# Performance work log

Measured on AMD Instinct MI355X. Metric: run time of the kernel, lower is better.

Reference implementation:

```python
import jax, jax.numpy as jnp
import numpy as np

N, B, M, C, NH, S, HC, T, OUT = 8, 256, 512, 512, 8, 8, 64, 3, 100
DH = C // NH


def setup_inputs() -> dict:
    key = jax.random.key(0)
    it = iter(jax.random.split(key, 40))
    def nrm(shape, s=0.02):
        return jax.random.normal(next(it), shape, jnp.float32) * s
    z = lambda shape: jnp.zeros(shape, jnp.float32)
    return {
        "x": jax.random.normal(next(it), (B, 3, 32, 32), jnp.float32),
        "conv1_w": nrm((N, 64, 3, 3, 3)), "conv1_b": z((N, 64)),
        "conv2_w": nrm((N, 128, 64, 3, 3)), "conv2_b": z((N, 128)),
        "feat_w": nrm((N, 128, M)), "feat_b": z((N, M)),
        "ctrl_wi": nrm((N, M, 3 * HC)), "ctrl_wh": nrm((N, HC, 3 * HC)),
        "ctrl_bi": z((N, 3 * HC)), "ctrl_bh": z((N, 3 * HC)),
        "send_w": nrm((N, HC, 1)), "send_b": z((N, 1)),
        "recv_w": nrm((N, HC, 1)), "recv_b": z((N, 1)),
        "abias_w": nrm((N, HC, NH)), "abias_b": z((N, NH)),
        "wq": nrm((N, M, C)), "wk": nrm((N, M, C)), "wv": nrm((N, M, C)),
        "wo": nrm((N, C, C)), "bo": z((N, C)),
        "edge_logits": nrm((N, N), 0.1),
        "wr": nrm((N, C, M)), "br": z((N, M)),
        "wg": nrm((N, 3 * M, M)), "bg": z((N, M)),
        "wc": nrm((N, 3 * M, M)), "bc": z((N, M)),
        "wcls": nrm((N, M, OUT)), "bcls": z((N, OUT)),
    }


def _forward(x, conv1_w, conv1_b, conv2_w, conv2_b, feat_w, feat_b,
             ctrl_wi, ctrl_wh, ctrl_bi, ctrl_bh,
             send_w, send_b, recv_w, recv_b, abias_w, abias_b,
             wq, wk, wv, wo, bo, edge_logits, wr, br,
             wg, bg, wc, bc, wcls, bcls):
    dn = ('NCHW', 'OIHW', 'NCHW')
    def conv(inp, w, b):
        y = jax.lax.conv_general_dilated(inp, w, (2, 2), 'SAME', dimension_numbers=dn)
        return jax.nn.relu(y + b[None, :, None, None])
    # per-node feature extraction (batched over N experts via vmap)
    h1 = jax.vmap(lambda w, b: conv(x, w, b))(conv1_w, conv1_b)          # [N,B,64,16,16]
    h2 = jax.vmap(conv, in_axes=(0, 0, 0))(h1, conv2_w, conv2_b)        # [N,B,128,8,8]
    pooled = h2.mean(axis=(-2, -1))                                      # [N,B,128]
    feats = jax.nn.relu(jnp.einsum('nbf,nfm->nbm', pooled, feat_w) + feat_b[:, None, :])
    h = feats                                                            # node states [N,B,M]
    cs = jnp.zeros((N, B, HC), x.dtype)                                  # controller GRU states
    buf = jnp.zeros((N, B, S, C), x.dtype)                               # message buffers
    scale = 1.0 / jnp.sqrt(jnp.asarray(DH, x.dtype))
    for t in range(T):
        # controller (GRUCell) -> send/recv gates + per-head attention bias
        gi = jnp.einsum('nbm,nmh->nbh', h, ctrl_wi) + ctrl_bi[:, None, :]
        gh = jnp.einsum('nbh,nhk->nbk', cs, ctrl_wh) + ctrl_bh[:, None, :]
        iz, ir, inn = jnp.split(gi, 3, -1)
        hz, hr, hn = jnp.split(gh, 3, -1)
        zg = jax.nn.sigmoid(iz + hz)
        rg = jax.nn.sigmoid(ir + hr)
        ng = jnp.tanh(inn + rg * hn)
        cs = (1.0 - zg) * ng + zg * cs
        send = jax.nn.sigmoid(jnp.einsum('nbh,nho->nbo', cs, send_w) + send_b[:, None, :])  # [N,B,1]
        recv = jax.nn.sigmoid(jnp.einsum('nbh,nho->nbo', cs, recv_w) + recv_b[:, None, :])  # [N,B,1]
        ab = jnp.einsum('nbh,nhk->nbk', cs, abias_w) + abias_b[:, None, :]                  # [N,B,NH]
        # per-node QKV
        q = jnp.einsum('nbm,nmc->nbc', h, wq).reshape(N, B, NH, DH)
        k = jnp.einsum('nbm,nmc->nbc', h, wk).reshape(N, B, NH, DH)
        v = jnp.einsum('nbm,nmc->nbc', h, wv).reshape(N, B, NH, DH)
        # graph-transformer attention over nodes: i=receiver, j=sender
        scores = jnp.einsum('ibhd,jbhd->ijbh', q, k) * scale
        scores = scores + edge_logits[:, :, None, None] + ab[:, None, :, :]
        attn = jax.nn.softmax(scores, axis=1)
        attn = attn * send[None, :, :, :] * recv[:, None, :, :]          # gated [N,N,B,NH]
        msg = jnp.einsum('ijbh,jbhd->ibhd', attn, v).reshape(N, B, C)
        msg = jnp.einsum('nbc,nck->nbk', msg, wo) + bo[:, None, :]
        # push into FIFO buffer, read out mean
        buf = jnp.concatenate([buf[:, :, 1:], msg[:, :, None, :]], axis=2)
        readout = jnp.einsum('nbc,ncm->nbm', buf.mean(axis=2), wr) + br[:, None, :]
        # gated state update fusing h, fresh features, buffer readout
        cat = jnp.concatenate([h, feats, readout], axis=-1)              # [N,B,3M]
        g = jax.nn.sigmoid(jnp.einsum('nbk,nkm->nbm', cat, wg) + bg[:, None, :])
        cand = jnp.tanh(jnp.einsum('nbk,nkm->nbm', cat, wc) + bc[:, None, :])
        h = (1.0 - g) * h + g * cand
    logits = jnp.einsum('nbm,nmo->nbo', h, wcls) + bcls[:, None, :]      # [N,B,OUT]
    return logits


def reference(x, conv1_w, conv1_b, conv2_w, conv2_b, feat_w, feat_b,
              ctrl_wi, ctrl_wh, ctrl_bi, ctrl_bh,
              send_w, send_b, recv_w, recv_b, abias_w, abias_b,
              wq, wk, wv, wo, bo, edge_logits, wr, br,
              wg, bg, wc, bc, wcls, bcls):
    return _forward(x, conv1_w, conv1_b, conv2_w, conv2_b, feat_w, feat_b,
                    ctrl_wi, ctrl_wh, ctrl_bi, ctrl_bh,
                    send_w, send_b, recv_w, recv_b, abias_w, abias_b,
                    wq, wk, wv, wo, bo, edge_logits, wr, br,
                    wg, bg, wc, bc, wcls, bcls)
```

## Files before the change

kernel.cpp:

```cpp
#include <hip/hip_runtime.h>
#include <hip/hip_bf16.h>


typedef _Float16 f16;
typedef _Float16 f16x8 __attribute__((ext_vector_type(8)));
typedef _Float16 f16x4 __attribute__((ext_vector_type(4)));
typedef _Float16 f16x2 __attribute__((ext_vector_type(2)));
typedef float f32x4 __attribute__((ext_vector_type(4)));

#define GLOAD_LDS16(gsrc, ldst)                                                   \
  __builtin_amdgcn_global_load_lds(                                               \
      (const __attribute__((address_space(1))) void*)(gsrc),                      \
      (__attribute__((address_space(3))) void*)(ldst), 16, 0, 0)

__device__ __forceinline__ void tw64_body(
    const float* __restrict__ s, f16* __restrict__ d, int K, int N, float scale,
    int n0, int k0, int t)
{
  __shared__ float tile[64][65];
#pragma unroll
  for (int p = 0; p < 4; p++) {
    int idx = t + p * 256;
    int kk = idx >> 4, nq = (idx & 15) * 4;
    float4 v = *(const float4*)&s[(long)(k0 + kk) * N + n0 + nq];
    tile[kk][nq] = v.x; tile[kk][nq + 1] = v.y; tile[kk][nq + 2] = v.z; tile[kk][nq + 3] = v.w;
  }
  __syncthreads();
#pragma unroll
  for (int p = 0; p < 2; p++) {
    int idx = t + p * 256;
    int nn = idx >> 3, kc = (idx & 7) * 8;
    f16 o[8];
#pragma unroll
    for (int i = 0; i < 8; i++) o[i] = (f16)(tile[kc + i][nn] * scale);
    *(f16x8*)&d[(long)(n0 + nn) * K + k0 + kc] = *(const f16x8*)o;
  }
}

__global__ __launch_bounds__(256) void tw64_kernel(
    const float* __restrict__ src, f16* __restrict__ dst, int K, int N, float scale)
{
  int z = blockIdx.z;
  tw64_body(src + (long)z * K * N, dst + (long)z * N * K, K, N, scale,
            blockIdx.x * 64, blockIdx.y * 64, threadIdx.x);
}

__global__ __launch_bounds__(256) void twmulti4_kernel(
    const float* __restrict__ wq, const float* __restrict__ wk,
    const float* __restrict__ wv, const float* __restrict__ wi, f16* __restrict__ wqT)
{
  int z = blockIdx.z, sel = z >> 3, e = z & 7;
  int N = (sel < 3) ? 512 : 192;
  int n0 = blockIdx.x * 64;
  if (n0 >= N) return;
  const float* src = (sel == 0) ? wq : (sel == 1) ? wk : (sel == 2) ? wv : wi;
  f16* dst = (sel < 3) ? (wqT + (long)sel * 2097152 + (long)e * 262144)
                       : (wqT + 3L * 2097152 + (long)e * 98304);
  tw64_body(src + (long)e * 512 * N, dst, 512, N, 1.f, n0, blockIdx.y * 64, threadIdx.x);
}

__global__ __launch_bounds__(256) void twmulti2_kernel(
    const float* __restrict__ wg, const float* __restrict__ wc, f16* __restrict__ wgT)
{
  int z = blockIdx.z, sel = z >> 3, e = z & 7;
  const float* src = sel ? wc : wg;
  f16* dst = wgT + (long)sel * 6291456 + (long)e * 786432;
  tw64_body(src + (long)e * 1536 * 512, dst, 1536, 512, 1.f,
            blockIdx.x * 64, blockIdx.y * 64, threadIdx.x);
}

__global__ __launch_bounds__(256) void clsprep_kernel(
    const float* __restrict__ wcls, f16* __restrict__ wclsT)
{
  __shared__ float tile[32][33];
  int e = blockIdx.z;
  int n0 = blockIdx.x * 32, k0 = blockIdx.y * 32;
  int tx = threadIdx.x & 31, ty = threadIdx.x >> 5;
  const float* s = wcls + (long)e * 51200;
  f16* d = wclsT + (long)e * 65536;
  for (int r = ty; r < 32; r += 8) {
    int k = k0 + r, n = n0 + tx;
    tile[r][tx] = (n < 100) ? s[(long)k * 100 + n] : 0.f;
  }
  __syncthreads();
  for (int r = ty; r < 32; r += 8) {
    int n = n0 + r, k = k0 + tx;
    d[(long)n * 512 + k] = (f16)tile[tx][r];
  }
}

__global__ __launch_bounds__(256) void smallprep_kernel(
    const float* __restrict__ wo, f16* __restrict__ wo16,
    const float* __restrict__ c2src, f16* __restrict__ c2dst,
    const float* __restrict__ w1src, f16* __restrict__ w1dst)
{
  int bid = blockIdx.x, t = threadIdx.x;
  if (bid < 1024) {
    long i = ((long)bid * 256 + t) * 8;
    float4 a = *(const float4*)&wo[i];
    float4 b = *(const float4*)&wo[i + 4];
    f16 o[8] = {(f16)a.x, (f16)a.y, (f16)a.z, (f16)a.w, (f16)b.x, (f16)b.y, (f16)b.z, (f16)b.w};
    *(f16x8*)&wo16[i] = *(const f16x8*)o;
  } else if (bid < 3328) {
    long i = (long)(bid - 1024) * 256 + t;
    int ci = i & 63; long r = i >> 6; int tap = r % 9; r /= 9; int co = r & 127; int n = (int)(r >> 7);
    c2dst[i] = (f16)c2src[(((long)(n * 128 + co) * 64 + ci) * 9) + tap];
  } else {
    int i = (bid - 3328) * 256 + t;
    int j = i & 7, co = (i >> 3) & 63, slot = (i >> 9) & 3, e = i >> 11;
    int k = slot * 8 + j;
    w1dst[i] = (f16)((k < 27) ? w1src[(long)e * 1728 + co * 27 + k] : 0.f);
  }
}

__global__ __launch_bounds__(256) void xprep_kernel(
    const float* __restrict__ x, f16* __restrict__ xp16)
{
  __shared__ float xs[3072];
  int b = blockIdx.x, t = threadIdx.x;
  const float* xb = x + (long)b * 3072;
  for (int i = t; i < 768; i += 256) ((float4*)xs)[i] = ((const float4*)xb)[i];
  __syncthreads();
  int oy = t >> 4, ox = t & 15;
  f16 pv[32];
#pragma unroll
  for (int q = 27; q < 32; q++) pv[q] = (f16)0.f;
#pragma unroll
  for (int ci = 0; ci < 3; ci++)
#pragma unroll
    for (int ky = 0; ky < 3; ky++) {
      int iy = oy * 2 + ky;
#pragma unroll
      for (int kx = 0; kx < 3; kx++) {
        int ix = ox * 2 + kx;
        pv[ci * 9 + ky * 3 + kx] =
            (f16)((iy < 32 && ix < 32) ? xs[ci * 1024 + iy * 32 + ix] : 0.f);
      }
    }
  f16* ob = xp16 + (long)b * 8192;
#pragma unroll
  for (int c = 0; c < 4; c++) *(f16x8*)&ob[c * 2048 + t * 8] = *(const f16x8*)&pv[c * 8];
}

__global__ __launch_bounds__(256) void borprep2_kernel(
    const f16* __restrict__ wrT, const float* __restrict__ bo, float* __restrict__ bor32)
{
  int n = blockIdx.y, t = threadIdx.x;
  int og = blockIdx.x * 16 + (t >> 4), k16 = t & 15;
  const f16* row = wrT + (long)n * 262144 + (long)og * 512 + k16 * 32;
  const float* bp = bo + n * 512 + k16 * 32;
  float s = 0.f;
#pragma unroll
  for (int i = 0; i < 32; i += 8) {
    f16x8 v = *(const f16x8*)&row[i];
    float4 b0 = *(const float4*)&bp[i];
    float4 b1 = *(const float4*)&bp[i + 4];
    s = fmaf((float)v[0], b0.x, s); s = fmaf((float)v[1], b0.y, s);
    s = fmaf((float)v[2], b0.z, s); s = fmaf((float)v[3], b0.w, s);
    s = fmaf((float)v[4], b1.x, s); s = fmaf((float)v[5], b1.y, s);
    s = fmaf((float)v[6], b1.z, s); s = fmaf((float)v[7], b1.w, s);
  }
  s += __shfl_xor(s, 1); s += __shfl_xor(s, 2);
  s += __shfl_xor(s, 4); s += __shfl_xor(s, 8);
  if (k16 == 0) bor32[n * 512 + og] = s;
}

__global__ __launch_bounds__(256) void biasfold2_kernel(
    const f16* __restrict__ wgT, const f16* __restrict__ wcT,
    const float* __restrict__ bg, const float* __restrict__ bc,
    const float* __restrict__ br, const float* __restrict__ bor32,
    float* __restrict__ bgr, float* __restrict__ vg2,
    float* __restrict__ bcr, float* __restrict__ vc2)
{
  int n = blockIdx.y, t = threadIdx.x;
  int og = blockIdx.x * 16 + (t >> 4), k16 = t & 15;
  const f16* gr = wgT + (long)n * 786432 + (long)og * 1536 + 1024 + k16 * 32;
  const f16* cr = wcT + (long)n * 786432 + (long)og * 1536 + 1024 + k16 * 32;
  const float* brp = br + n * 512 + k16 * 32;
  const float* bop = bor32 + n * 512 + k16 * 32;
  float s1g = 0.f, s2g = 0.f, s1c = 0.f, s2c = 0.f;
#pragma unroll
  for (int i = 0; i < 32; i += 8) {
    f16x8 gv = *(const f16x8*)&gr[i];
    f16x8 cv = *(const f16x8*)&cr[i];
#pragma unroll
    for (int q = 0; q < 8; q++) {
      float brm = brp[i + q], bom = bop[i + q];
      s1g = fmaf(brm, (float)gv[q], s1g); s2g = fmaf(bom, (float)gv[q], s2g);
      s1c = fmaf(brm, (float)cv[q], s1c); s2c = fmaf(bom, (float)cv[q], s2c);
    }
  }
#pragma unroll
  for (int o = 1; o < 16; o <<= 1) {
    s1g += __shfl_xor(s1g, o); s2g += __shfl_xor(s2g, o);
    s1c += __shfl_xor(s1c, o); s2c += __shfl_xor(s2c, o);
  }
  if (k16 == 0) {
    bgr[n * 512 + og] = bg[n * 512 + og] + s1g; vg2[n * 512 + og] = s2g;
    bcr[n * 512 + og] = bc[n * 512 + og] + s1c; vc2[n * 512 + og] = s2c;
  }
}

__global__ __launch_bounds__(256) void convfused_kernel(
    const f16* __restrict__ xp16, const f16* __restrict__ w1p, const float* __restrict__ b1,
    const f16* __restrict__ w2p, const float* __restrict__ b2, f16* __restrict__ pooled16)
{
  __shared__ __align__(16) char lds[53632];
  f16* xpatch = (f16*)lds;
  f16* AsubS = (f16*)lds;
  float* red = (float*)lds;
  float* bs1 = (float*)(lds + 16384);
  f16* h1s = (f16*)(lds + 16640);
  f16* ws1 = (f16*)(lds + 16640);

  int b = blockIdx.x, e = blockIdx.y;
  int t = threadIdx.x, w = t >> 6, l = t & 63;

  const f16* xb = xp16 + (long)b * 8192;
#pragma unroll
  for (int c = 0; c < 4; c++)
    GLOAD_LDS16(xb + (w * 4 + c) * 512 + l * 8, &xpatch[(w * 4 + c) * 512]);
  GLOAD_LDS16(w1p + (long)e * 2048 + w * 512 + l * 8, &ws1[w * 512]);
  if (t < 64) bs1[t] = b1[e * 64 + t];
  asm volatile("s_waitcnt vmcnt(0)" ::: "memory");
  __syncthreads();

  {
    int pw = w * 64;
    f16x8 a1[4], b1f[4];
#pragma unroll
    for (int i = 0; i < 4; i++)
      a1[i] = *(const f16x8*)&ws1[(l >> 4) * 512 + (i * 16 + (l & 15)) * 8];
#pragma unroll
    for (int jj = 0; jj < 4; jj++)
      b1f[jj] = *(const f16x8*)&xpatch[(l >> 4) * 2048 + (pw + jj * 16 + (l & 15)) * 8];
    __syncthreads();
    f32x4 acc1[4][4];
#pragma unroll
    for (int i = 0; i < 4; i++)
#pragma unroll
      for (int jj = 0; jj < 4; jj++)
        acc1[i][jj] = __builtin_amdgcn_mfma_f32_16x16x32_f16(
            a1[i], b1f[jj], (f32x4){0.f, 0.f, 0.f, 0.f}, 0, 0, 0);
#pragma unroll
    for (int i = 0; i < 4; i++) {
      int co0 = i * 16 + ((l >> 4) << 2);
      float bi0 = bs1[co0], bi1 = bs1[co0 + 1], bi2 = bs1[co0 + 2], bi3 = bs1[co0 + 3];
#pragma unroll
      for (int jj = 0; jj < 4; jj++) {
        int p2 = pw + jj * 16 + (l & 15);
        int oy2 = p2 >> 4, ox2 = p2 & 15;
        int p = oy2 * 17 + ox2;
        int fs = ((ox2 >> 1) + oy2) & 7;
        int slot = (co0 >> 3) ^ fs;
        f16x4 v;
        v[0] = (f16)fmaxf(acc1[i][jj][0] + bi0, 0.f);
        v[1] = (f16)fmaxf(acc1[i][jj][1] + bi1, 0.f);
        v[2] = (f16)fmaxf(acc1[i][jj][2] + bi2, 0.f);
        v[3] = (f16)fmaxf(acc1[i][jj][3] + bi3, 0.f);
        *(f16x4*)&h1s[p * 64 + slot * 8 + (co0 & 7)] = v;
      }
    }
  }
  if (t < 33) {
    int gy = (t < 17) ? 16 : (t - 17);
    int gx = (t < 17) ? t : 16;
    int p = gy * 17 + gx;
    f16x8 zz = {};
#pragma unroll
    for (int g = 0; g < 8; g++) *(f16x8*)&h1s[p * 64 + g * 8] = zz;
  }

  int waveR = w >> 1, waveC = w & 1;
  const f16* wbase = w2p + (long)e * 73728;
  f32x4 acc[4][2];
#pragma unroll
  for (int i = 0; i < 4; i++) {
    acc[i][0] = (f32x4){0.f, 0.f, 0.f, 0.f};
    acc[i][1] = (f32x4){0.f, 0.f, 0.f, 0.f};
  }
  for (int tap = 0; tap < 9; tap++) {
    __syncthreads();
#pragma unroll
    for (int c = 0; c < 4; c++) {
      int ch = w * 4 + c;
      int co = ch * 8 + (l >> 3);
      int g = (l & 7) ^ (co & 7);
      GLOAD_LDS16(wbase + ((long)co * 9 + tap) * 64 + g * 8, &AsubS[ch * 512]);
    }
    asm volatile("s_waitcnt vmcnt(0)" ::: "memory");
    __syncthreads();
    int ky = tap / 3, kx = tap - ky * 3;
#pragma unroll
    for (int kk = 0; kk < 2; kk++) {
      f16x8 af[4], bf[2];
#pragma unroll
      for (int i = 0; i < 4; i++) {
        int row = waveR * 64 + i * 16 + (l & 15);
        int blk = (kk * 4 + (l >> 4)) ^ (row & 7);
        af[i] = *(const f16x8*)&AsubS[row * 64 + blk * 8];
      }
#pragma unroll
      for (int j = 0; j < 2; j++) {
        int sp = waveC * 32 + j * 16 + (l & 15);
        int iy = (sp >> 3) * 2 + ky, ix = (sp & 7) * 2 + kx;
        int fs = ((ix >> 1) + iy) & 7;
        int blk = (kk * 4 + (l >> 4)) ^ fs;
        bf[j] = *(const f16x8*)&h1s[(iy * 17 + ix) * 64 + blk * 8];
      }
#pragma unroll
      for (int i = 0; i < 4; i++)
#pragma unroll
        for (int j = 0; j < 2; j++)
          acc[i][j] = __builtin_amdgcn_mfma_f32_16x16x32_f16(af[i], bf[j], acc[i][j], 0, 0, 0);
    }
  }
  __syncthreads();
  const float* bn2 = b2 + e * 128;
#pragma unroll
  for (int i = 0; i < 4; i++) {
#pragma unroll
    for (int reg = 0; reg < 4; reg++) {
      int row = waveR * 64 + i * 16 + ((l >> 4) << 2) + reg;
      float bi = bn2[row];
      float s = fmaxf(acc[i][0][reg] + bi, 0.f) + fmaxf(acc[i][1][reg] + bi, 0.f);
      s += __shfl_xor(s, 1); s += __shfl_xor(s, 2);
      s += __shfl_xor(s, 4); s += __shfl_xor(s, 8);
      if ((l & 15) == 0) red[waveC * 128 + row] = s;
    }
  }
  __syncthreads();
  if (t < 128) {
    float v = (red[t] + red[128 + t]) * (1.f / 64.f);
    pooled16[((long)e * 256 + b) * 128 + t] = (f16)v;
  }
}

struct SegsM {
  const f16* BT[4];
  const float* bias[4];
  f16* o16[4];
  f16* o16b[4];
  float* o32[4];
  long sBT[4], sBias[4], sO16[4], sO32[4];
  int ldo16[4], ldo32[4], act[4], segCols[4];
};

template <int MR>
__global__ __launch_bounds__(256) void gemmf16_kernel(
    const f16* __restrict__ A, long sA, int lda, SegsM segs, int K)
{
  constexpr int IW = MR / 32;
  __shared__ __align__(16) f16 Asub[2][MR * 64];
  __shared__ __align__(16) f16 Bsub[2][4096];
  int z = blockIdx.z;
  int rowBase = blockIdx.y * MR;
  int vcBase = blockIdx.x * 64;
  int seg = vcBase >> 9;
  int lcBase = vcBase & 511;
  const f16* An = A + (long)z * sA + (long)rowBase * lda;
  const f16* BTn = segs.BT[seg] + (long)z * segs.sBT[seg] + (long)lcBase * K;
  const float* biasN = segs.bias[seg] ? segs.bias[seg] + (long)z * segs.sBias[seg] : nullptr;
  int act = segs.act[seg];
  int segCols = segs.segCols[seg];
  int t = threadIdx.x, w = t >> 6, l = t & 63;
  int waveR = w >> 1, waveC = w & 1;
  f32x4 acc[IW][2];
#pragma unroll
  for (int i = 0; i < IW; i++) {
    acc[i][0] = (f32x4){0.f, 0.f, 0.f, 0.f};
    acc[i][1] = (f32x4){0.f, 0.f, 0.f, 0.f};
  }
  auto stage = [&](int buf, int kt) {
    int k0 = kt << 6;
#pragma unroll
    for (int c = 0; c < MR / 32; c++) {
      int ch = w * (MR / 32) + c;
      int row = ch * 8 + (l >> 3);
      int g = (l & 7) ^ (row & 7);
      GLOAD_LDS16(An + (long)row * lda + k0 + g * 8, &Asub[buf][ch * 512]);
    }
#pragma unroll
    for (int c = 0; c < 2; c++) {
      int ch = w * 2 + c;
      int col = ch * 8 + (l >> 3);
      int g = (l & 7) ^ (col & 7);
      GLOAD_LDS16(BTn + (long)col * K + k0 + g * 8, &Bsub[buf][ch * 512]);
    }
  };
  int nk = K >> 6;
  stage(0, 0);
  asm volatile("s_waitcnt vmcnt(0)" ::: "memory");
  __syncthreads();
  int cur = 0;
  for (int kt = 0; kt < nk; kt++) {
    if (kt + 1 < nk) stage(cur ^ 1, kt + 1);
#pragma unroll
    for (int kk = 0; kk < 2; kk++) {
      f16x8 af[IW], bf[2];
#pragma unroll
      for (int i = 0; i < IW; i++) {
        int row = waveR * (MR / 2) + i * 16 + (l & 15);
        int blk = (kk * 4 + (l >> 4)) ^ (row & 7);
        af[i] = *(const f16x8*)&Asub[cur][row * 64 + blk * 8];
      }
#pragma unroll
      for (int j = 0; j < 2; j++) {
        int col = waveC * 32 + j * 16 + (l & 15);
        int blk = (kk * 4 + (l >> 4)) ^ (col & 7);
        bf[j] = *(const f16x8*)&Bsub[cur][col * 64 + blk * 8];
      }
#pragma unroll
      for (int i = 0; i < IW; i++)
#pragma unroll
        for (int j = 0; j < 2; j++)
          acc[i][j] = __builtin_amdgcn_mfma_f32_16x16x32_f16(af[i], bf[j], acc[i][j], 0, 0, 0);
    }
    if (kt + 1 < nk) {
      asm volatile("s_waitcnt vmcnt(0)" ::: "memory");
      __syncthreads();
      cur ^= 1;
    }
  }
  f16* o16 = segs.o16[seg];
  f16* o16b = segs.o16b[seg];
  float* o32 = segs.o32[seg];
  long sO16 = segs.sO16[seg], sO32 = segs.sO32[seg];
  int ldo16 = segs.ldo16[seg], ldo32 = segs.ldo32[seg];
#pragma unroll
  for (int i = 0; i < IW; i++) {
    int rb = rowBase + waveR * (MR / 2) + i * 16 + ((l >> 4) << 2);
#pragma unroll
    for (int j = 0; j < 2; j++) {
      int lc = lcBase + waveC * 32 + j * 16 + (l & 15);
      if (lc >= segCols) continue;
      float bv = biasN ? biasN[lc] : 0.f;
#pragma unroll
      for (int reg = 0; reg < 4; reg++) {
        float v = acc[i][j][reg] + bv;
        if (act == 1) v = fmaxf(v, 0.f);
        else if (act == 2) v = 1.f / (1.f + __expf(-v));
        else if (act == 3) v = tanhf(v);
        long rr = rb + reg;
        if (o16) o16[(long)z * sO16 + rr * ldo16 + lc] = (f16)v;
        if (o16b) o16b[(long)z * sO16 + rr * ldo16 + lc] = (f16)v;
        if (o32) o32[(long)z * sO32 + rr * ldo32 + lc] = v;
      }
    }
  }
}

__global__ __launch_bounds__(256) void step_kernel(
    const f16* __restrict__ qkv16, const float* __restrict__ gi32,
    const float* __restrict__ wh, const float* __restrict__ bh,
    float* __restrict__ cs, const float* __restrict__ sw, const float* __restrict__ sb,
    const float* __restrict__ rw, const float* __restrict__ rb,
    const float* __restrict__ aw, const float* __restrict__ abb,
    const float* __restrict__ edge,
    float* __restrict__ msgsum32, f16* __restrict__ msgsum16, int step)
{
  int b = blockIdx.x, t = threadIdx.x;
  __shared__ float qs[8 * 520], ks[8 * 520];
  __shared__ f16 vs16[8 * 520];
  __shared__ float csh[512];
  __shared__ float sc[512];
  __shared__ float se[8], re[8], edg[64], abl[64];

  for (int i = t; i < 2048; i += 256) {
    int nn = i >> 8, c2 = (i & 255) * 2;
    int h = c2 >> 6, d = c2 & 63;
    long base = ((long)nn * 256 + b) * 1536 + c2;
    int la = nn * 520 + h * 65 + d;
    f16x2 qv = *(const f16x2*)&qkv16[base];
    f16x2 kv = *(const f16x2*)&qkv16[base + 512];
    *(f16x2*)&vs16[la] = *(const f16x2*)&qkv16[base + 1024];
    qs[la] = (float)qv[0]; qs[la + 1] = (float)qv[1];
    ks[la] = (float)kv[0]; ks[la + 1] = (float)kv[1];
  }
  if (t >= 192) edg[t - 192] = edge[t - 192];
  int n0 = t >> 6, hc = t & 63;
  if (step > 0) {
    csh[t] = cs[((long)n0 * 256 + b) * 64 + hc];
    csh[t + 256] = cs[((long)(n0 + 4) * 256 + b) * 64 + hc];
  }
  __syncthreads();

  float cn[2];
#pragma unroll
  for (int u = 0; u < 2; u++) {
    int n = n0 + u * 4;
    long nb = (long)n * 256 + b;
    float c0 = (step > 0) ? csh[n * 64 + hc] : 0.f;
    float g0 = bh[n * 192 + hc], g1 = bh[n * 192 + 64 + hc], g2 = bh[n * 192 + 128 + hc];
    if (step > 0) {
      const float* whn = wh + (long)n * 12288;
      for (int k = 0; k < 64; k++) {
        float cv = csh[n * 64 + k];
        g0 = fmaf(cv, whn[k * 192 + hc], g0);
        g1 = fmaf(cv, whn[k * 192 + 64 + hc], g1);
        g2 = fmaf(cv, whn[k * 192 + 128 + hc], g2);
      }
    }
    const float* gi = gi32 + nb * 192;
    float zg = 1.f / (1.f + __expf(-(gi[hc] + g0)));
    float rg = 1.f / (1.f + __expf(-(gi[64 + hc] + g1)));
    float ng = tanhf(gi[128 + hc] + rg * g2);
    cn[u] = (1.f - zg) * ng + zg * c0;
    cs[nb * 64 + hc] = cn[u];
  }
#pragma unroll
  for (int u = 0; u < 2; u++) {
    int n = n0 + u * 4;
    float ps = cn[u] * sw[n * 64 + hc];
    float pr = cn[u] * rw[n * 64 + hc];
#pragma unroll
    for (int o = 32; o; o >>= 1) { ps += __shfl_xor(ps, o); pr += __shfl_xor(pr, o); }
    if (hc == 0) {
      se[n] = 1.f / (1.f + __expf(-(ps + sb[n])));
      re[n] = 1.f / (1.f + __expf(-(pr + rb[n])));
    }
#pragma unroll
    for (int kk = 0; kk < 8; kk++) {
      float pa = cn[u] * aw[(n * 64 + hc) * 8 + kk];
#pragma unroll
      for (int o = 32; o; o >>= 1) pa += __shfl_xor(pa, o);
      if (hc == 0) abl[n * 8 + kk] = pa + abb[n * 8 + kk];
    }
  }
  __syncthreads();

  for (int idx = t; idx < 512; idx += 256) {
    int i = idx >> 6, j = (idx >> 3) & 7, h = idx & 7;
    const float* qp = &qs[i * 520 + h * 65];
    const float* kp = &ks[j * 520 + h * 65];
    float s = 0.f;
#pragma unroll
    for (int d = 0; d < 64; d++) s = fmaf(qp[d], kp[d], s);
    sc[idx] = s * 0.125f + edg[i * 8 + j] + abl[i * 8 + h];
  }
  __syncthreads();
  if (t < 64) {
    int i = t >> 3, h = t & 7;
    float mx = -1e30f;
#pragma unroll
    for (int j = 0; j < 8; j++) mx = fmaxf(mx, sc[(i << 6) + (j << 3) + h]);
    float e[8], sm = 0.f;
#pragma unroll
    for (int j = 0; j < 8; j++) { e[j] = __expf(sc[(i << 6) + (j << 3) + h] - mx); sm += e[j]; }
    float inv = re[i] / sm;
#pragma unroll
    for (int j = 0; j < 8; j++) sc[(i << 6) + (j << 3) + h] = e[j] * inv * se[j];
  }
  __syncthreads();
  for (int idx = t; idx < 4096; idx += 256) {
    int i = idx >> 9, c = idx & 511, h = c >> 6, d = c & 63;
    float s = 0.f;
#pragma unroll
    for (int j = 0; j < 8; j++)
      s = fmaf(sc[(i << 6) + (j << 3) + h], (float)vs16[j * 520 + h * 65 + d], s);
    long oi = ((long)i * 256 + b) * 512 + c;
    float nv = (step == 0) ? s : (msgsum32[oi] + s);
    msgsum32[oi] = nv;
    msgsum16[oi] = (f16)nv;
  }
}

__global__ __launch_bounds__(256) void gatefused_kernel(
    const f16* __restrict__ h16cur, const f16* __restrict__ feats16,
    const f16* __restrict__ msgsum16,
    const f16* __restrict__ wgT, const f16* __restrict__ wcT,
    const f16* __restrict__ WeffGT, const f16* __restrict__ WeffCT,
    const float* __restrict__ bgr, const float* __restrict__ vg2,
    const float* __restrict__ bcr, const float* __restrict__ vc2,
    float* __restrict__ h32, f16* __restrict__ h16next, float tp1)
{
  __shared__ __align__(16) f16 Asub[2][2048];
  __shared__ __align__(16) f16 Bgs[2][4096];
  __shared__ __align__(16) f16 Bcs[2][4096];
  int z = blockIdx.z;
  int rowBase = blockIdx.y * 32;
  int colBase = blockIdx.x * 64;
  int t = threadIdx.x, w = t >> 6, l = t & 63;
  int waveR = w >> 1, waveC = w & 1;
  f32x4 accG[2], accC[2];
  accG[0] = (f32x4){0.f, 0.f, 0.f, 0.f}; accG[1] = accG[0];
  accC[0] = accG[0]; accC[1] = accG[0];

  auto stage = [&](int buf, int kt) {
    {
      const f16* asrc;
      if (kt < 8)       asrc = h16cur  + (long)z * 131072 + kt * 64;
      else if (kt < 16) asrc = feats16 + (long)z * 131072 + (kt - 8) * 64;
      else              asrc = msgsum16 + (long)z * 131072 + (kt - 16) * 64;
      int row = w * 8 + (l >> 3);
      int g = (l & 7) ^ (row & 7);
      GLOAD_LDS16(asrc + (long)(rowBase + row) * 512 + g * 8, &Asub[buf][w * 512]);
    }
#pragma unroll
    for (int c = 0; c < 2; c++) {
      int ch = w * 2 + c;
      int cl = ch * 8 + (l >> 3);
      int g = (l & 7) ^ (cl & 7);
      const f16 *bgsrc, *bcsrc;
      if (kt < 16) {
        bgsrc = wgT + (long)z * 786432 + (long)(colBase + cl) * 1536 + kt * 64 + g * 8;
        bcsrc = wcT + (long)z * 786432 + (long)(colBase + cl) * 1536 + kt * 64 + g * 8;
      } else {
        bgsrc = WeffGT + (long)z * 262144 + (long)(colBase + cl) * 512 + (kt - 16) * 64 + g * 8;
        bcsrc = WeffCT + (long)z * 262144 + (long)(colBase + cl) * 512 + (kt - 16) * 64 + g * 8;
      }
      GLOAD_LDS16(bgsrc, &Bgs[buf][ch * 512]);
      GLOAD_LDS16(bcsrc, &Bcs[buf][ch * 512]);
    }
  };
  stage(0, 0);
  asm volatile("s_waitcnt vmcnt(0)" ::: "memory");
  __syncthreads();
  int cur = 0;
  for (int kt = 0; kt < 24; kt++) {
    if (kt + 1 < 24) stage(cur ^ 1, kt + 1);
#pragma unroll
    for (int kk = 0; kk < 2; kk++) {
      f16x8 af, bgf[2], bcf[2];
      {
        int row = waveR * 16 + (l & 15);
        int blk = (kk * 4 + (l >> 4)) ^ (row & 7);
        af = *(const f16x8*)&Asub[cur][row * 64 + blk * 8];
      }
#pragma unroll
      for (int j = 0; j < 2; j++) {
        int cl = waveC * 32 + j * 16 + (l & 15);
        int blk = (kk * 4 + (l >> 4)) ^ (cl & 7);
        bgf[j] = *(const f16x8*)&Bgs[cur][cl * 64 + blk * 8];
        bcf[j] = *(const f16x8*)&Bcs[cur][cl * 64 + blk * 8];
      }
#pragma unroll
      for (int j = 0; j < 2; j++) {
        accG[j] = __builtin_amdgcn_mfma_f32_16x16x32_f16(af, bgf[j], accG[j], 0, 0, 0);
        accC[j] = __builtin_amdgcn_mfma_f32_16x16x32_f16(af, bcf[j], accC[j], 0, 0, 0);
      }
    }
    if (kt + 1 < 24) {
      asm volatile("s_waitcnt vmcnt(0)" ::: "memory");
      __syncthreads();
      cur ^= 1;
    }
  }
#pragma unroll
  for (int j = 0; j < 2; j++) {
    int col = colBase + waveC * 32 + j * 16 + (l & 15);
    float bG = bgr[z * 512 + col] + tp1 * vg2[z * 512 + col];
    float bC = bcr[z * 512 + col] + tp1 * vc2[z * 512 + col];
#pragma unroll
    for (int reg = 0; reg < 4; reg++) {
      int row = rowBase + waveR * 16 + ((l >> 4) << 2) + reg;
      float g = 1.f / (1.f + __expf(-(accG[j][reg] + bG)));
      float cd = tanhf(accC[j][reg] + bC);
      long hidx = ((long)z * 256 + row) * 512 + col;
      float h = h32[hidx];
      float nh = (1.f - g) * h + g * cd;
      h32[hidx] = nh;
      h16next[hidx] = (f16)nh;
    }
  }
}

extern "C" void kernel_launch(void* const* d_in, const int* in_sizes, int n_in,
                              void* d_out, int out_size, void* d_ws, size_t ws_size,
                              hipStream_t stream)
{
  (void)in_sizes; (void)n_in; (void)out_size;
  const float* x        = (const float*)d_in[0];
  const float* conv1_w  = (const float*)d_in[1];
  const float* conv1_b  = (const float*)d_in[2];
  const float* conv2_w  = (const float*)d_in[3];
  const float* conv2_b  = (const float*)d_in[4];
  const float* feat_w   = (const float*)d_in[5];
  const float* feat_b   = (const float*)d_in[6];
  const float* ctrl_wi  = (const float*)d_in[7];
  const float* ctrl_wh  = (const float*)d_in[8];
  const float* ctrl_bi  = (const float*)d_in[9];
  const float* ctrl_bh  = (const float*)d_in[10];
  const float* send_w   = (const float*)d_in[11];
  const float* send_b   = (const float*)d_in[12];
  const float* recv_w   = (const float*)d_in[13];
  const float* recv_b   = (const float*)d_in[14];
  const float* abias_w  = (const float*)d_in[15];
  const float* abias_b  = (const float*)d_in[16];
  const float* wq       = (const float*)d_in[17];
  const float* wk       = (const float*)d_in[18];
  const float* wv       = (const float*)d_in[19];
  const float* wo       = (const float*)d_in[20];
  const float* bo       = (const float*)d_in[21];
  const float* edge     = (const float*)d_in[22];
  const float* wr       = (const float*)d_in[23];
  const float* br       = (const float*)d_in[24];
  const float* wg       = (const float*)d_in[25];
  const float* bg       = (const float*)d_in[26];
  const float* wc       = (const float*)d_in[27];
  const float* bc       = (const float*)d_in[28];
  const float* wcls     = (const float*)d_in[29];
  const float* bcls     = (const float*)d_in[30];

  float* f32b = (float*)d_ws;
  float* h32      = f32b;
  float* gi32     = f32b + 1048576;
  float* msgsum32 = f32b + 1441792;
  float* cs       = f32b + 2490368;
  float* bor32    = f32b + 2621440;
  float* bgr      = f32b + 2625536;
  float* vg2b     = f32b + 2629632;
  float* bcr      = f32b + 2633728;
  float* vc2b     = f32b + 2637824;
  f16* hb = (f16*)(f32b + 2641920);
  f16* pooled16 = hb;
  f16* h16a     = hb + 262144;
  f16* h16b     = hb + 1310720;
  f16* feats16  = hb + 2359296;
  f16* msgsum16 = hb + 3407872;
  f16* qkv16    = hb + 4456448;
  f16* wqT      = hb + 7602176;
  f16* wiT      = hb + 13893632;
  f16* featwT   = hb + 14680064;
  f16* wrT      = hb + 15204352;
  f16* wgT      = hb + 17301504;
  f16* wcT      = hb + 23592960;
  f16* c2wp     = hb + 29884416;
  f16* wo16     = hb + 30474240;
  f16* P        = hb + 32571392;
  f16* P2       = hb + 34668544;
  f16* WeffGT   = hb + 36765696;
  f16* WeffCT   = hb + 38862848;
  f16* w1p      = hb + 40960000;
  f16* xp16     = hb + 40976384;
  f16* wclsT    = hb + 43073536;
  if (ws_size < 97763328ull) return;

  f16* hbuf[2] = {h16a, h16b};

  twmulti4_kernel<<<dim3(8, 8, 32), 256, 0, stream>>>(wq, wk, wv, ctrl_wi, wqT);
  twmulti2_kernel<<<dim3(8, 24, 16), 256, 0, stream>>>(wg, wc, wgT);
  tw64_kernel<<<dim3(8, 8, 8), 256, 0, stream>>>(wr, wrT, 512, 512, 0.125f);
  tw64_kernel<<<dim3(8, 2, 8), 256, 0, stream>>>(feat_w, featwT, 128, 512, 1.f);
  smallprep_kernel<<<3392, 256, 0, stream>>>(wo, wo16, conv2_w, c2wp, conv1_w, w1p);
  xprep_kernel<<<256, 256, 0, stream>>>(x, xp16);
  clsprep_kernel<<<dim3(4, 16, 8), 256, 0, stream>>>(wcls, wclsT);
  borprep2_kernel<<<dim3(32, 8), 256, 0, stream>>>(wrT, bo, bor32);
  biasfold2_kernel<<<dim3(32, 8), 256, 0, stream>>>(wgT, wcT, bg, bc, br, bor32,
                                                    bgr, vg2b, bcr, vc2b);
  {
    SegsM s{};
    s.BT[0] = wrT; s.sBT[0] = 262144;
    s.o16[0] = P; s.o16b[0] = P2; s.sO16[0] = 262144; s.ldo16[0] = 512;
    s.segCols[0] = 512;
    gemmf16_kernel<64><<<dim3(8, 8, 8), 256, 0, stream>>>(wo16, 262144L, 512, s, 512);
  }
  {
    SegsM s{};
    s.BT[0] = P; s.sBT[0] = 262144;
    s.o16[0] = WeffGT; s.sO16[0] = 262144; s.ldo16[0] = 512;
    s.segCols[0] = 512;
    gemmf16_kernel<64><<<dim3(8, 8, 16), 256, 0, stream>>>(wgT + 1024, 786432L, 1536, s, 512);
  }

  convfused_kernel<<<dim3(256, 8), 256, 0, stream>>>(xp16, w1p, conv1_b, c2wp, conv2_b, pooled16);

  {
    SegsM s{};
    s.BT[0] = featwT; s.sBT[0] = 65536; s.bias[0] = feat_b; s.sBias[0] = 512; s.act[0] = 1;
    s.o16[0] = feats16; s.o16b[0] = h16a; s.sO16[0] = 131072; s.ldo16[0] = 512;
    s.o32[0] = h32; s.sO32[0] = 131072; s.ldo32[0] = 512;
    s.segCols[0] = 512;
    gemmf16_kernel<128><<<dim3(8, 2, 8), 256, 0, stream>>>(pooled16, 32768L, 128, s, 128);
  }

  for (int step = 0; step < 3; step++) {
    {
      SegsM s{};
      s.BT[0] = wqT;            s.sBT[0] = 262144;
      s.BT[1] = wqT + 2097152;  s.sBT[1] = 262144;
      s.BT[2] = wqT + 4194304;  s.sBT[2] = 262144;
      s.BT[3] = wiT;            s.sBT[3] = 98304;
      s.bias[3] = ctrl_bi; s.sBias[3] = 192;
      s.o16[0] = qkv16;        s.sO16[0] = 393216; s.ldo16[0] = 1536;
      s.o16[1] = qkv16 + 512;  s.sO16[1] = 393216; s.ldo16[1] = 1536;
      s.o16[2] = qkv16 + 1024; s.sO16[2] = 393216; s.ldo16[2] = 1536;
      s.o32[3] = gi32; s.sO32[3] = 49152; s.ldo32[3] = 192;
      s.segCols[0] = 512; s.segCols[1] = 512; s.segCols[2] = 512; s.segCols[3] = 192;
      gemmf16_kernel<128><<<dim3(27, 2, 8), 256, 0, stream>>>(hbuf[step & 1], 131072L, 512, s, 512);
    }
    step_kernel<<<256, 256, 0, stream>>>(
        qkv16, gi32, ctrl_wh, ctrl_bh, cs, send_w, send_b, recv_w, recv_b,
        abias_w, abias_b, edge, msgsum32, msgsum16, step);
    gatefused_kernel<<<dim3(8, 8, 8), 256, 0, stream>>>(
        hbuf[step & 1], feats16, msgsum16, wgT, wcT, WeffGT, WeffCT,
        bgr, vg2b, bcr, vc2b, h32, hbuf[(step + 1) & 1], (float)(step + 1));
  }
  {
    SegsM s{};
    s.BT[0] = wclsT; s.sBT[0] = 65536;
    s.bias[0] = bcls; s.sBias[0] = 100;
    s.o32[0] = (float*)d_out; s.sO32[0] = 25600; s.ldo32[0] = 100;
    s.segCols[0] = 100;
    gemmf16_kernel<128><<<dim3(2, 2, 8), 256, 0, stream>>>(hbuf[1], 131072L, 512, s, 512);
  }
}
```

Baseline: 324.2 us.

## Split conv2 output channels across blocks and triple-buffer weight taps

The fused conv kernel now launches twice as many blocks, each computing 64 of the 128 conv2 output channels and recomputing conv1 for its image. Conv1 weights and input are read straight from global into registers instead of through LDS. Conv2 weight taps are triple-buffered in LDS with partial vmcnt waits, so the next taps load while the current one computes, and there is one barrier per tap instead of two. This trades doubled conv1 work for more parallelism and load/compute overlap, with a larger LDS footprint per block.

```diff
diff --git a/kernel.cpp b/kernel.cpp
--- a/kernel.cpp
+++ b/kernel.cpp
@@ -205,36 +205,40 @@
     const f16* __restrict__ xp16, const f16* __restrict__ w1p, const float* __restrict__ b1,
     const f16* __restrict__ w2p, const float* __restrict__ b2, f16* __restrict__ pooled16)
 {
-  __shared__ __align__(16) char lds[53632];
-  f16* xpatch = (f16*)lds;
-  f16* AsubS = (f16*)lds;
+  __shared__ __align__(16) char lds[61568];
+  f16* Asub = (f16*)lds;
   float* red = (float*)lds;
-  float* bs1 = (float*)(lds + 16384);
-  f16* h1s = (f16*)(lds + 16640);
-  f16* ws1 = (f16*)(lds + 16640);
-
-  int b = blockIdx.x, e = blockIdx.y;
+  f16* h1s = (f16*)(lds + 24576);
+
+  int b = blockIdx.x, e = blockIdx.y, ch2 = blockIdx.z;
   int t = threadIdx.x, w = t >> 6, l = t & 63;
-
-  const f16* xb = xp16 + (long)b * 8192;
-#pragma unroll
-  for (int c = 0; c < 4; c++)
-    GLOAD_LDS16(xb + (w * 4 + c) * 512 + l * 8, &xpatch[(w * 4 + c) * 512]);
-  GLOAD_LDS16(w1p + (long)e * 2048 + w * 512 + l * 8, &ws1[w * 512]);
-  if (t < 64) bs1[t] = b1[e * 64 + t];
-  asm volatile("s_waitcnt vmcnt(0)" ::: "memory");
-  __syncthreads();
+  int waveR = w >> 1, waveC = w & 1;
+
+  const f16* wsg = w1p + (long)e * 2048;
+  const f16* xg = xp16 + (long)b * 8192;
+  int pw = w * 64;
+  f16x8 a1[4], b1f[4];
+#pragma unroll
+  for (int i = 0; i < 4; i++)
+    a1[i] = *(const f16x8*)&wsg[(l >> 4) * 512 + (i * 16 + (l & 15)) * 8];
+#pragma unroll
+  for (int jj = 0; jj < 4; jj++)
+    b1f[jj] = *(const f16x8*)&xg[(l >> 4) * 2048 + (pw + jj * 16 + (l & 15)) * 8];
+
+  const f16* wbase = w2p + (long)e * 73728 + (long)ch2 * 36864;
+  auto stageA = [&](int buf, int tap) {
+#pragma unroll
+    for (int c = 0; c < 2; c++) {
+      int ch = w * 2 + c;
+      int row = ch * 8 + (l >> 3);
+      int g = (l & 7) ^ (row & 7);
+      GLOAD_LDS16(wbase + (long)row * 576 + tap * 64 + g * 8, &Asub[buf * 4096 + ch * 512]);
+    }
+  };
+  stageA(0, 0);
+  stageA(1, 1);
 
   {
-    int pw = w * 64;
-    f16x8 a1[4], b1f[4];
-#pragma unroll
-    for (int i = 0; i < 4; i++)
-      a1[i] = *(const f16x8*)&ws1[(l >> 4) * 512 + (i * 16 + (l & 15)) * 8];
-#pragma unroll
-    for (int jj = 0; jj < 4; jj++)
-      b1f[jj] = *(const f16x8*)&xpatch[(l >> 4) * 2048 + (pw + jj * 16 + (l & 15)) * 8];
-    __syncthreads();
     f32x4 acc1[4][4];
 #pragma unroll
     for (int i = 0; i < 4; i++)
@@ -245,7 +249,7 @@
 #pragma unroll
     for (int i = 0; i < 4; i++) {
       int co0 = i * 16 + ((l >> 4) << 2);
-      float bi0 = bs1[co0], bi1 = bs1[co0 + 1], bi2 = bs1[co0 + 2], bi3 = bs1[co0 + 3];
+      float4 bv = *(const float4*)&b1[e * 64 + co0];
 #pragma unroll
       for (int jj = 0; jj < 4; jj++) {
         int p2 = pw + jj * 16 + (l & 15);
@@ -254,10 +258,10 @@
         int fs = ((ox2 >> 1) + oy2) & 7;
         int slot = (co0 >> 3) ^ fs;
         f16x4 v;
-        v[0] = (f16)fmaxf(acc1[i][jj][0] + bi0, 0.f);
-        v[1] = (f16)fmaxf(acc1[i][jj][1] + bi1, 0.f);
-        v[2] = (f16)fmaxf(acc1[i][jj][2] + bi2, 0.f);
-        v[3] = (f16)fmaxf(acc1[i][jj][3] + bi3, 0.f);
+        v[0] = (f16)fmaxf(acc1[i][jj][0] + bv.x, 0.f);
+        v[1] = (f16)fmaxf(acc1[i][jj][1] + bv.y, 0.f);
+        v[2] = (f16)fmaxf(acc1[i][jj][2] + bv.z, 0.f);
+        v[3] = (f16)fmaxf(acc1[i][jj][3] + bv.w, 0.f);
         *(f16x4*)&h1s[p * 64 + slot * 8 + (co0 & 7)] = v;
       }
     }
@@ -270,35 +274,30 @@
 #pragma unroll
     for (int g = 0; g < 8; g++) *(f16x8*)&h1s[p * 64 + g * 8] = zz;
   }
-
-  int waveR = w >> 1, waveC = w & 1;
-  const f16* wbase = w2p + (long)e * 73728;
-  f32x4 acc[4][2];
-#pragma unroll
-  for (int i = 0; i < 4; i++) {
-    acc[i][0] = (f32x4){0.f, 0.f, 0.f, 0.f};
-    acc[i][1] = (f32x4){0.f, 0.f, 0.f, 0.f};
-  }
+  asm volatile("s_waitcnt lgkmcnt(0)" ::: "memory");
+  __builtin_amdgcn_s_barrier();
+  asm volatile("" ::: "memory");
+
+  f32x4 acc[2][2];
+  acc[0][0] = (f32x4){0.f, 0.f, 0.f, 0.f}; acc[0][1] = acc[0][0];
+  acc[1][0] = acc[0][0]; acc[1][1] = acc[0][0];
+#pragma unroll
   for (int tap = 0; tap < 9; tap++) {
-    __syncthreads();
-#pragma unroll
-    for (int c = 0; c < 4; c++) {
-      int ch = w * 4 + c;
-      int co = ch * 8 + (l >> 3);
-      int g = (l & 7) ^ (co & 7);
-      GLOAD_LDS16(wbase + ((long)co * 9 + tap) * 64 + g * 8, &AsubS[ch * 512]);
-    }
-    asm volatile("s_waitcnt vmcnt(0)" ::: "memory");
-    __syncthreads();
-    int ky = tap / 3, kx = tap - ky * 3;
+    if (tap < 8) { asm volatile("s_waitcnt vmcnt(2)" ::: "memory"); }
+    else         { asm volatile("s_waitcnt vmcnt(0)" ::: "memory"); }
+    __builtin_amdgcn_s_barrier();
+    asm volatile("" ::: "memory");
+    if (tap + 2 <= 8) stageA((tap + 2) % 3, tap + 2);
+    const int ky = tap / 3, kx = tap - ky * 3;
+    const f16* Ab = &Asub[(tap % 3) * 4096];
 #pragma unroll
     for (int kk = 0; kk < 2; kk++) {
-      f16x8 af[4], bf[2];
-#pragma unroll
-      for (int i = 0; i < 4; i++) {
-        int row = waveR * 64 + i * 16 + (l & 15);
+      f16x8 af[2], bf[2];
+#pragma unroll
+      for (int i = 0; i < 2; i++) {
+        int row = waveR * 32 + i * 16 + (l & 15);
         int blk = (kk * 4 + (l >> 4)) ^ (row & 7);
-        af[i] = *(const f16x8*)&AsubS[row * 64 + blk * 8];
+        af[i] = *(const f16x8*)&Ab[row * 64 + blk * 8];
       }
 #pragma unroll
       for (int j = 0; j < 2; j++) {
@@ -309,30 +308,31 @@
         bf[j] = *(const f16x8*)&h1s[(iy * 17 + ix) * 64 + blk * 8];
       }
 #pragma unroll
-      for (int i = 0; i < 4; i++)
+      for (int i = 0; i < 2; i++)
 #pragma unroll
         for (int j = 0; j < 2; j++)
           acc[i][j] = __builtin_amdgcn_mfma_f32_16x16x32_f16(af[i], bf[j], acc[i][j], 0, 0, 0);
     }
   }
-  __syncthreads();
-  const float* bn2 = b2 + e * 128;
-#pragma unroll
-  for (int i = 0; i < 4; i++) {
+  const float* bn2 = b2 + e * 128 + ch2 * 64;
+#pragma unroll
+  for (int i = 0; i < 2; i++) {
 #pragma unroll
     for (int reg = 0; reg < 4; reg++) {
-      int row = waveR * 64 + i * 16 + ((l >> 4) << 2) + reg;
+      int row = waveR * 32 + i * 16 + ((l >> 4) << 2) + reg;
       float bi = bn2[row];
       float s = fmaxf(acc[i][0][reg] + bi, 0.f) + fmaxf(acc[i][1][reg] + bi, 0.f);
       s += __shfl_xor(s, 1); s += __shfl_xor(s, 2);
       s += __shfl_xor(s, 4); s += __shfl_xor(s, 8);
-      if ((l & 15) == 0) red[waveC * 128 + row] = s;
-    }
-  }
-  __syncthreads();
-  if (t < 128) {
-    float v = (red[t] + red[128 + t]) * (1.f / 64.f);
-    pooled16[((long)e * 256 + b) * 128 + t] = (f16)v;
+      if ((l & 15) == 0) red[waveC * 64 + row] = s;
+    }
+  }
+  asm volatile("s_waitcnt lgkmcnt(0)" ::: "memory");
+  __builtin_amdgcn_s_barrier();
+  asm volatile("" ::: "memory");
+  if (t < 64) {
+    float v = (red[t] + red[64 + t]) * (1.f / 64.f);
+    pooled16[((long)e * 256 + b) * 128 + ch2 * 64 + t] = (f16)v;
   }
 }
 
@@ -763,7 +763,7 @@
     gemmf16_kernel<64><<<dim3(8, 8, 16), 256, 0, stream>>>(wgT + 1024, 786432L, 1536, s, 512);
   }
 
-  convfused_kernel<<<dim3(256, 8), 256, 0, stream>>>(xp16, w1p, conv1_b, c2wp, conv2_b, pooled16);
+  convfused_kernel<<<dim3(256, 8, 2), 256, 0, stream>>>(xp16, w1p, conv1_b, c2wp, conv2_b, pooled16);
 
   {
     SegsM s{};
```

Measured after the change: 338.6 us. 1.04x slower.
